# Optimization experiments

Hardware: AMD Instinct MI355X
Metric: run time of the kernel (lower is better)

The kernel has to match this reference:

```python
import jax, jax.numpy as jnp
import numpy as np

B, N = 32, 128
V, P, L = 50000, 40, 50
WD, UD = 100, 25
D = WD + UD          # 125: LSTM hidden per direction
H2 = 2 * D           # 250: BiLSTM output
HID = 100            # hidden_dim for scorers


def setup_inputs() -> dict:
    key = jax.random.key(0)
    ks = iter(jax.random.split(key, 40))
    p = lambda shape: jax.random.normal(next(ks), shape, jnp.float32) * 0.05
    inp = {
        'word_ids': jax.random.randint(next(ks), (B, N), 0, V),
        'upos_ids': jax.random.randint(next(ks), (B, N), 0, P),
        'target_arcs': jax.random.randint(next(ks), (B, N), 0, N),
        'wlookup': p((V, WD)),
        'tlookup': p((V, UD)),  # original sizes tag table by word_count
        # LSTM layer 0 (input D=125), layer 1 (input 2D=250); f=fwd, b=bwd dir
        'l0f_Wih': p((4 * D, D)), 'l0f_Whh': p((4 * D, D)), 'l0f_b': p((4 * D,)),
        'l0b_Wih': p((4 * D, D)), 'l0b_Whh': p((4 * D, D)), 'l0b_b': p((4 * D,)),
        'l1f_Wih': p((4 * D, H2)), 'l1f_Whh': p((4 * D, D)), 'l1f_b': p((4 * D,)),
        'l1b_Wih': p((4 * D, H2)), 'l1b_Whh': p((4 * D, D)), 'l1b_b': p((4 * D,)),
        'eh_W': p((HID, H2)), 'eh_b': p((HID,)),
        'em_W': p((HID, H2)), 'em_b': p((HID,)),
        'es_W': p((1, HID)), 'es_b': p((1,)),
        'lh_W': p((HID, H2)), 'lh_b': p((HID,)),
        'lm_W': p((HID, H2)), 'lm_b': p((HID,)),
        'ls_W': p((L, HID)), 'ls_b': p((L,)),
    }
    return inp


def _lstm_dir(x, Wih, Whh, b, reverse):
    # x: [B,T,in] -> h: [B,T,H], pytorch gate order i,f,g,o
    H = Whh.shape[1]
    xg = jnp.einsum('bti,gi->btg', x, Wih) + b  # precompute input projections

    def step(carry, xt):
        h, c = carry
        g = xt + h @ Whh.T
        i, f, gg, o = jnp.split(g, 4, axis=-1)
        c = jax.nn.sigmoid(f) * c + jax.nn.sigmoid(i) * jnp.tanh(gg)
        h = jax.nn.sigmoid(o) * jnp.tanh(c)
        return (h, c), h

    h0 = jnp.zeros((x.shape[0], H), x.dtype)
    _, hs = jax.lax.scan(step, (h0, h0), jnp.swapaxes(xg, 0, 1), reverse=reverse)
    return jnp.swapaxes(hs, 0, 1)


def _bilstm(x, Wf, Uf, bf, Wb, Ub, bb):
    return jnp.concatenate([_lstm_dir(x, Wf, Uf, bf, False),
                            _lstm_dir(x, Wb, Ub, bb, True)], axis=-1)


def reference(word_ids, upos_ids, target_arcs, wlookup, tlookup,
              l0f_Wih, l0f_Whh, l0f_b, l0b_Wih, l0b_Whh, l0b_b,
              l1f_Wih, l1f_Whh, l1f_b, l1b_Wih, l1b_Whh, l1b_b,
              eh_W, eh_b, em_W, em_b, es_W, es_b,
              lh_W, lh_b, lm_W, lm_b, ls_W, ls_b):
    n = word_ids.shape[1]
    words = jnp.concatenate([wlookup[word_ids], tlookup[upos_ids]], axis=-1)  # [B,N,125]
    h0 = _bilstm(words, l0f_Wih, l0f_Whh, l0f_b, l0b_Wih, l0b_Whh, l0b_b)
    word_exprs = _bilstm(h0, l1f_Wih, l1f_Whh, l1f_b, l1b_Wih, l1b_Whh, l1b_b)  # [B,N,250]

    word_h = word_exprs @ eh_W.T + eh_b  # [B,N,100]
    word_m = word_exprs @ em_W.T + em_b
    # fused pairwise biaffine-style scoring (replaces the O(n) python loop)
    pair = jnp.tanh(word_h[:, :, None, :] + word_m[:, None, :, :])  # [B,N,N,100]
    arc_scores = jnp.einsum('bijh,h->bij', pair, es_W[0]) + es_b[0]  # [B,N,N]

    # training path: margin augmentation
    target_arcs = target_arcs.at[:, 0].set(0)
    margin = 1.0 - jax.nn.one_hot(target_arcs, n, dtype=arc_scores.dtype)
    arc_scores = arc_scores + margin

    # decode() is an external MST decoder; greedy argmax stand-in
    parsed_trees = jnp.argmax(arc_scores, axis=-1)

    tree = target_arcs  # is_train path
    rel_heads = jnp.take_along_axis(word_exprs, tree[:, :, None], axis=1)  # [B,N,250]
    rel_heads = rel_heads @ lh_W.T + lh_b
    rel_mod = word_exprs @ lm_W.T + lm_b
    rel_scores = jnp.tanh(rel_mod + rel_heads) @ ls_W.T + ls_b  # [B,N,L]
    predicted_rels = jnp.argmax(rel_scores, axis=-1)
    return (parsed_trees, predicted_rels, arc_scores, rel_scores)
```

## Files before the change

### kernel.cpp

```cpp
#include <hip/hip_runtime.h>
#include <hip/hip_bf16.h>
#include <math.h>

#define B 32
#define N 128
#define BT (B*N)
#define WD 100
#define UD 25
#define D 125
#define G4 (4*D)
#define H2 (2*D)
#define HID 100
#define L 50

__device__ __forceinline__ float fast_tanh(float x) {
    float e = __expf(2.0f * x);
    return 1.0f - 2.0f / (e + 1.0f);
}
__device__ __forceinline__ float fast_sigmoid(float x) {
    return 1.0f / (1.0f + __expf(-x));
}
__device__ __forceinline__ float bcast_lane(float v, int k) {
    return __builtin_bit_cast(float, __builtin_amdgcn_readlane(__builtin_bit_cast(int, v), k));
}

#define REP64(X) \
 X(0) X(1) X(2) X(3) X(4) X(5) X(6) X(7) X(8) X(9) \
 X(10) X(11) X(12) X(13) X(14) X(15) X(16) X(17) X(18) X(19) \
 X(20) X(21) X(22) X(23) X(24) X(25) X(26) X(27) X(28) X(29) \
 X(30) X(31) X(32) X(33) X(34) X(35) X(36) X(37) X(38) X(39) \
 X(40) X(41) X(42) X(43) X(44) X(45) X(46) X(47) X(48) X(49) \
 X(50) X(51) X(52) X(53) X(54) X(55) X(56) X(57) X(58) X(59) \
 X(60) X(61) X(62) X(63)

struct TJob { const float* src; float* dst; int R, C, ldo, coff, tile0, tiles_x; };
struct TArgs { TJob j[12]; };

__global__ __launch_bounds__(256)
void setup_fused(TArgs a, int n_tr,
                 const int* __restrict__ wids, const int* __restrict__ uids,
                 const float* __restrict__ wl, const float* __restrict__ tl,
                 float* __restrict__ words,
                 const float* __restrict__ l0f_b, const float* __restrict__ l0b_b,
                 const float* __restrict__ l1f_b, const float* __restrict__ l1b_b,
                 const float* __restrict__ eh_b, const float* __restrict__ em_b,
                 const float* __restrict__ lm_b,
                 float* __restrict__ b_l0, float* __restrict__ b_l1,
                 float* __restrict__ b_s3,
                 float* __restrict__ p0, float* __restrict__ p1,
                 float* __restrict__ p2, float* __restrict__ p3) {
    __shared__ float tile[32][33];
    int bid = blockIdx.x;
    int tid = threadIdx.x;
    if (bid < n_tr) {
        int ji = 0;
        #pragma unroll
        for (int i = 1; i < 12; i++) if (bid >= a.j[i].tile0) ji = i;
        TJob jb = a.j[ji];
        int t = bid - jb.tile0;
        int tx = t % jb.tiles_x, ty = t / jb.tiles_x;
        int txx = tid & 31, tyy = tid >> 5;
        int k0 = tx*32, n0 = ty*32;
        #pragma unroll
        for (int dy = 0; dy < 32; dy += 8) {
            int n = n0 + tyy + dy, k = k0 + txx;
            if (n < jb.R && k < jb.C)
                tile[tyy+dy][txx] = jb.src[(size_t)n*jb.C + k];
        }
        __syncthreads();
        #pragma unroll
        for (int dy = 0; dy < 32; dy += 8) {
            int k = k0 + tyy + dy, n = n0 + txx;
            if (k < jb.C && n < jb.R)
                jb.dst[(size_t)k*jb.ldo + jb.coff + n] = tile[txx][tyy+dy];
        }
        return;
    }
    bid -= n_tr;
    if (bid < 2048) {
        int bt = bid*2 + (tid >> 7);
        int t = tid & 127;
        int wid = wids[bt], uid = uids[bt];
        if (t < WD)       words[bt*D + t] = wl[(size_t)wid*WD + t];
        else if (t < D)   words[bt*D + t] = tl[(size_t)uid*UD + (t - WD)];
        return;
    }
    bid -= 2048;
    if (bid < 9) {
        int t = bid*256 + tid;
        if (t < 500)        b_l0[t] = l0f_b[t];
        else if (t < 1000)  b_l0[t] = l0b_b[t-500];
        else if (t < 1500)  b_l1[t-1000] = l1f_b[t-1000];
        else if (t < 2000)  b_l1[t-1000] = l1b_b[t-1500];
        else if (t < 2100)  b_s3[t-2000] = eh_b[t-2000];
        else if (t < 2200)  b_s3[t-2000] = em_b[t-2100];
        else if (t < 2300)  b_s3[t-2000] = lm_b[t-2200];
        return;
    }
    bid -= 9;
    int e = bid*256 + tid;
    if (e < 6064) {
        int m = e / 1516, o = e % 1516;
        float* p = (m == 0) ? p0 : (m == 1) ? p1 : (m == 2) ? p2 : p3;
        p[125*500 + o] = 0.0f;
    }
}

#define MT 16
template<int CPT, int BD>
__device__ __forceinline__
void proj_body(const float* __restrict__ x, const float* __restrict__ WT,
               const float* __restrict__ bias, float* __restrict__ out,
               int Ncols, int K, int ldx, const int* __restrict__ gather_idx,
               int blk, float* xs) {
    int m0 = blk * MT;
    for (int e = threadIdx.x; e < MT * K; e += BD) {
        int r = e / K, k = e - r * K;
        int m = m0 + r;
        int row = m;
        if (gather_idx) {
            int bb = m >> 7, np = m & 127;
            row = (bb << 7) + (np == 0 ? 0 : gather_idx[m]);
        }
        xs[k*17 + r] = x[(size_t)row*ldx + k];
    }
    __syncthreads();
    int n0 = threadIdx.x;
    int lane = threadIdx.x & 63;
    float acc[CPT][MT];
    int ncl[CPT];
    #pragma unroll
    for (int j = 0; j < CPT; j++) {
        int n = n0 + j*BD;
        ncl[j] = (n < Ncols) ? n : (Ncols - 1);
        #pragma unroll
        for (int r = 0; r < MT; r++) acc[j][r] = 0.0f;
    }
    float wkc[4][CPT];
    #pragma unroll
    for (int q = 0; q < 4; q++)
        #pragma unroll
        for (int j = 0; j < CPT; j++)
            wkc[q][j] = WT[(size_t)q*Ncols + ncl[j]];
    int k0 = 0;
    for (; k0 + 8 <= K; k0 += 4) {
        float xv = xs[(k0 + (lane >> 4))*17 + (lane & 15)];
        float wkn[4][CPT];
        #pragma unroll
        for (int q = 0; q < 4; q++)
            #pragma unroll
            for (int j = 0; j < CPT; j++)
                wkn[q][j] = WT[(size_t)(k0 + 4 + q)*Ncols + ncl[j]];
        #pragma unroll
        for (int q = 0; q < 4; q++) {
            #pragma unroll
            for (int r = 0; r < 16; r++) {
                float hv = bcast_lane(xv, q*16 + r);
                #pragma unroll
                for (int j = 0; j < CPT; j++)
                    acc[j][r] = fmaf(wkc[q][j], hv, acc[j][r]);
            }
        }
        #pragma unroll
        for (int q = 0; q < 4; q++)
            #pragma unroll
            for (int j = 0; j < CPT; j++)
                wkc[q][j] = wkn[q][j];
    }
    {
        float xv = xs[(k0 + (lane >> 4))*17 + (lane & 15)];
        #pragma unroll
        for (int q = 0; q < 4; q++) {
            #pragma unroll
            for (int r = 0; r < 16; r++) {
                float hv = bcast_lane(xv, q*16 + r);
                #pragma unroll
                for (int j = 0; j < CPT; j++)
                    acc[j][r] = fmaf(wkc[q][j], hv, acc[j][r]);
            }
        }
        k0 += 4;
    }
    for (; k0 < K; k0++) {
        float xv = xs[k0*17 + (lane & 15)];
        float wk[CPT];
        #pragma unroll
        for (int j = 0; j < CPT; j++) wk[j] = WT[(size_t)k0*Ncols + ncl[j]];
        #pragma unroll
        for (int r = 0; r < 16; r++) {
            float hv = bcast_lane(xv, r);
            #pragma unroll
            for (int j = 0; j < CPT; j++)
                acc[j][r] = fmaf(wk[j], hv, acc[j][r]);
        }
    }
    #pragma unroll
    for (int j = 0; j < CPT; j++) {
        int n = n0 + j*BD;
        if (n < Ncols) {
            float bb = bias[n];
            #pragma unroll
            for (int r = 0; r < MT; r++) out[(size_t)(m0 + r)*Ncols + n] = acc[j][r] + bb;
        }
    }
}

__global__ __launch_bounds__(512)
void proj_t(const float* __restrict__ x, const float* __restrict__ WT,
            const float* __restrict__ bias, float* __restrict__ out,
            int Ncols, int K, int ldx) {
    __shared__ float xs[250 * 17 + 16];
    proj_body<2, 512>(x, WT, bias, out, Ncols, K, ldx, nullptr, blockIdx.x, xs);
}

__global__ __launch_bounds__(256)
void proj_s3lh(const float* __restrict__ x,
               const float* __restrict__ WTa, const float* __restrict__ ba,
               float* __restrict__ outa,
               const float* __restrict__ WTb, const float* __restrict__ bb,
               float* __restrict__ outb, const int* __restrict__ gather_idx) {
    __shared__ float xs[250 * 17 + 16];
    int job = blockIdx.x >> 8;
    int blk = blockIdx.x & 255;
    if (job == 0)
        proj_body<2, 256>(x, WTa, ba, outa, 300, H2, H2, nullptr, blk, xs);
    else
        proj_body<2, 256>(x, WTb, bb, outb, 100, H2, H2, gather_idx, blk, xs);
}

__global__ __launch_bounds__(1024, 4)
void lstm_scan(const float* __restrict__ xgc,
               const float* __restrict__ WhTf, const float* __restrict__ WhTb,
               float* __restrict__ out) {
    int dir = blockIdx.x & 1;
    int b = blockIdx.x >> 1;
    const float* WhT = dir ? WhTb : WhTf;
    int off = dir ? D : 0;
    int t = threadIdx.x;
    int g = t & 511;
    int half = t >> 9;
    int kbase = half << 6;

    __shared__ __align__(16) float hbuf[128];
    __shared__ float pbuf[1024];

    unsigned voff0 = ((unsigned)kbase * 500u + (unsigned)g) * 4u;
#define DECLW(i) float w##i; \
    asm volatile("global_load_dword %0, %1, %2" \
                 : "=v"(w##i) : "v"(voff0 + (unsigned)(i)*2000u), "s"(WhT));
    REP64(DECLW)
#undef DECLW
    asm volatile("s_waitcnt vmcnt(0)" ::: "memory");

    float c = 0.0f;
    if (t < 128) hbuf[t] = 0.0f;
    __syncthreads();

    const float* xb = xgc + (size_t)b * N * 1000 + dir * 500;
    bool xa = (half == 0) && (g < G4);
    float x_next = xa ? xb[(size_t)(dir ? (N-1) : 0) * 1000 + g] : 0.0f;

    const float4* h4q = ((const float4*)hbuf) + (kbase >> 2);

#define FMA4(q, i0, i1, i2, i3) { float4 hv = h4q[q]; \
    a4[0] = fmaf(w##i0, hv.x, a4[0]); \
    a4[1] = fmaf(w##i1, hv.y, a4[1]); \
    a4[2] = fmaf(w##i2, hv.z, a4[2]); \
    a4[3] = fmaf(w##i3, hv.w, a4[3]); }

    for (int ti = 0; ti < N; ti++) {
        int tt = dir ? (N-1-ti) : ti;
        float x_cur = x_next;
        float xn = 0.0f;
        if (xa && ti + 1 < N)
            xn = xb[(size_t)(dir ? (tt-1) : (tt+1)) * 1000 + g];
        float a4[4];
        a4[0] = x_cur; a4[1] = 0.0f; a4[2] = 0.0f; a4[3] = 0.0f;
        FMA4(0,  0,  1,  2,  3)  FMA4(1,  4,  5,  6,  7)
        FMA4(2,  8,  9, 10, 11)  FMA4(3, 12, 13, 14, 15)
        FMA4(4, 16, 17, 18, 19)  FMA4(5, 20, 21, 22, 23)
        FMA4(6, 24, 25, 26, 27)  FMA4(7, 28, 29, 30, 31)
        FMA4(8, 32, 33, 34, 35)  FMA4(9, 36, 37, 38, 39)
        FMA4(10, 40, 41, 42, 43) FMA4(11, 44, 45, 46, 47)
        FMA4(12, 48, 49, 50, 51) FMA4(13, 52, 53, 54, 55)
        FMA4(14, 56, 57, 58, 59) FMA4(15, 60, 61, 62, 63)
        x_next = xn;
        pbuf[t] = (a4[0] + a4[1]) + (a4[2] + a4[3]);
        __syncthreads();
        if (t < D) {
            float iv = pbuf[t]       + pbuf[512 + t];
            float fv = pbuf[D+t]     + pbuf[512 + D+t];
            float gv = pbuf[2*D+t]   + pbuf[512 + 2*D+t];
            float ov = pbuf[3*D+t]   + pbuf[512 + 3*D+t];
            float si = fast_sigmoid(iv);
            float sf = fast_sigmoid(fv);
            float so = fast_sigmoid(ov);
            c = sf * c + si * fast_tanh(gv);
            float h = so * fast_tanh(c);
            hbuf[t] = h;
            out[(size_t)(b*N + tt)*H2 + off + t] = h;
        }
        __syncthreads();
    }
#undef FMA4
}

#define ITILE 4
__global__ __launch_bounds__(128)
void arc_rel(const float* __restrict__ s3,
             const float* __restrict__ esW, const float* __restrict__ esb,
             const int* __restrict__ ta, const float* __restrict__ rh,
             const float* __restrict__ lsW, const float* __restrict__ lsb,
             float* __restrict__ arc_out, float* __restrict__ tree_out,
             float* __restrict__ rel_out, float* __restrict__ pred_out) {
    __shared__ float wms[128 * 101];
    __shared__ float whs[ITILE][HID];
    __shared__ float es[HID];
    __shared__ float sv[128];
    __shared__ int   si[128];
    int j = threadIdx.x;

    if (blockIdx.x < 1024) {
        int blk = blockIdx.x;
        int b = blk >> 5, it = blk & 31;
        for (int e = j; e < 128 * HID; e += 128) {
            int r = e / HID, h = e - r * HID;
            wms[r*101 + h] = s3[(size_t)(b*N + r)*300 + 100 + h];
        }
        for (int e = j; e < ITILE * HID; e += 128) {
            int ii = e / HID, h = e - ii * HID;
            whs[ii][h] = s3[(size_t)(b*N + it*ITILE + ii)*300 + h];
        }
        if (j < HID) es[j] = esW[j];
        __syncthreads();
        float eb = esb[0];
        const float* wmr = &wms[j * 101];
        for (int ii = 0; ii < ITILE; ii++) {
            int i = it * ITILE + ii;
            int bi = b * N + i;
            float acc = 0.0f;
            for (int h = 0; h < HID; h++)
                acc = fmaf(es[h], fast_tanh(whs[ii][h] + wmr[h]), acc);
            int tai = (i == 0) ? 0 : ta[bi];
            float score = acc + eb + 1.0f - ((j == tai) ? 1.0f : 0.0f);
            arc_out[(size_t)bi*N + j] = score;
            sv[j] = score; si[j] = j;
            __syncthreads();
            for (int s = 64; s; s >>= 1) {
                if (j < s) {
                    float ov = sv[j+s]; int oi = si[j+s];
                    if (ov > sv[j] || (ov == sv[j] && oi < si[j])) { sv[j] = ov; si[j] = oi; }
                }
                __syncthreads();
            }
            if (j == 0) tree_out[bi] = (float)si[0];
            __syncthreads();
        }
    } else {
        int bt = blockIdx.x - 1024;
        float* tv = es;
        if (j < HID)
            tv[j] = fast_tanh(s3[(size_t)bt*300 + 200 + j] + rh[(size_t)bt*HID + j]);
        __syncthreads();
        float score = -1e30f;
        if (j < L) {
            float acc = 0.0f;
            const float* wrow = lsW + j*HID;
            for (int h = 0; h < HID; h++) acc = fmaf(wrow[h], tv[h], acc);
            score = acc + lsb[j];
            rel_out[(size_t)bt*L + j] = score;
        }
        sv[j] = score; si[j] = j;
        __syncthreads();
        for (int s = 64; s; s >>= 1) {
            if (j < s) {
                float ov = sv[j+s]; int oi = si[j+s];
                if (ov > sv[j] || (ov == sv[j] && oi < si[j])) { sv[j] = ov; si[j] = oi; }
            }
            __syncthreads();
        }
        if (j == 0) pred_out[bt] = (float)si[0];
    }
}

extern "C" void kernel_launch(void* const* d_in, const int* in_sizes, int n_in,
                              void* d_out, int out_size, void* d_ws, size_t ws_size,
                              hipStream_t stream) {
    const int*   word_ids    = (const int*)  d_in[0];
    const int*   upos_ids    = (const int*)  d_in[1];
    const int*   target_arcs = (const int*)  d_in[2];
    const float* wlookup     = (const float*)d_in[3];
    const float* tlookup     = (const float*)d_in[4];
    const float* l0f_Wih = (const float*)d_in[5];
    const float* l0f_Whh = (const float*)d_in[6];
    const float* l0f_b   = (const float*)d_in[7];
    const float* l0b_Wih = (const float*)d_in[8];
    const float* l0b_Whh = (const float*)d_in[9];
    const float* l0b_b   = (const float*)d_in[10];
    const float* l1f_Wih = (const float*)d_in[11];
    const float* l1f_Whh = (const float*)d_in[12];
    const float* l1f_b   = (const float*)d_in[13];
    const float* l1b_Wih = (const float*)d_in[14];
    const float* l1b_Whh = (const float*)d_in[15];
    const float* l1b_b   = (const float*)d_in[16];
    const float* eh_W = (const float*)d_in[17];
    const float* eh_b = (const float*)d_in[18];
    const float* em_W = (const float*)d_in[19];
    const float* em_b = (const float*)d_in[20];
    const float* es_W = (const float*)d_in[21];
    const float* es_b = (const float*)d_in[22];
    const float* lh_W = (const float*)d_in[23];
    const float* lh_b = (const float*)d_in[24];
    const float* lm_W = (const float*)d_in[25];
    const float* lm_b = (const float*)d_in[26];
    const float* ls_W = (const float*)d_in[27];
    const float* ls_b = (const float*)d_in[28];

    float* out = (float*)d_out;
    float* trees_out = out;
    float* preds_out = out + BT;
    float* arc_out   = out + 2*BT;
    float* rel_out   = out + 2*BT + BT*N;

    float* ws = (float*)d_ws;
    float* A       = ws;
    float* words   = ws + 4096000;
    float* C       = ws + 4608000;
    float* WT_l0   = ws + 5632000;
    float* WT_l1   = ws + 5757000;
    float* WT_s3   = ws + 6007000;
    float* WT_lh   = ws + 6082000;
    float* WhT_l0f = ws + 6107000;
    float* WhT_l0b = ws + 6171016;
    float* WhT_l1f = ws + 6235032;
    float* WhT_l1b = ws + 6299048;
    float* b_l0    = ws + 6363064;
    float* b_l1    = ws + 6364064;
    float* b_s3    = ws + 6365064;
    float* rel_head = ws + 6366064;

    TArgs ta{};
    int n_tr = 0;
    {
        auto tiles = [](int R, int C_) { return ((C_+31)/32) * ((R+31)/32); };
        struct { const float* s; float* d; int R, C, ldo, coff; } js[12] = {
            { l0f_Wih, WT_l0, 500, 125, 1000, 0 },
            { l0b_Wih, WT_l0, 500, 125, 1000, 500 },
            { l1f_Wih, WT_l1, 500, 250, 1000, 0 },
            { l1b_Wih, WT_l1, 500, 250, 1000, 500 },
            { eh_W, WT_s3, 100, 250, 300, 0 },
            { em_W, WT_s3, 100, 250, 300, 100 },
            { lm_W, WT_s3, 100, 250, 300, 200 },
            { lh_W, WT_lh, 100, 250, 100, 0 },
            { l0f_Whh, WhT_l0f, 500, 125, 500, 0 },
            { l0b_Whh, WhT_l0b, 500, 125, 500, 0 },
            { l1f_Whh, WhT_l1f, 500, 125, 500, 0 },
            { l1b_Whh, WhT_l1b, 500, 125, 500, 0 },
        };
        for (int i = 0; i < 12; i++) {
            ta.j[i].src = js[i].s;  ta.j[i].dst = js[i].d;
            ta.j[i].R = js[i].R;    ta.j[i].C = js[i].C;
            ta.j[i].ldo = js[i].ldo; ta.j[i].coff = js[i].coff;
            ta.j[i].tile0 = n_tr;
            ta.j[i].tiles_x = (js[i].C + 31) / 32;
            n_tr += tiles(js[i].R, js[i].C);
        }
    }
    setup_fused<<<n_tr + 2048 + 9 + 24, 256, 0, stream>>>(
        ta, n_tr, word_ids, upos_ids, wlookup, tlookup, words,
        l0f_b, l0b_b, l1f_b, l1b_b, eh_b, em_b, lm_b,
        b_l0, b_l1, b_s3, WhT_l0f, WhT_l0b, WhT_l1f, WhT_l1b);

    proj_t<<<BT/MT, 512, 0, stream>>>(words, WT_l0, b_l0, A, 1000, D, D);

    lstm_scan<<<B*2, 1024, 0, stream>>>(A, WhT_l0f, WhT_l0b, C);

    proj_t<<<BT/MT, 512, 0, stream>>>(C, WT_l1, b_l1, A, 1000, H2, H2);

    lstm_scan<<<B*2, 1024, 0, stream>>>(A, WhT_l1f, WhT_l1b, C);

    proj_s3lh<<<512, 256, 0, stream>>>(C, WT_s3, b_s3, A,
                                       WT_lh, lh_b, rel_head, target_arcs);

    arc_rel<<<1024 + BT, 128, 0, stream>>>(A, es_W, es_b, target_arcs, rel_head,
                                           ls_W, ls_b, arc_out, trees_out,
                                           rel_out, preds_out);
}
```

Baseline: 594.2 us.

## Restructure LSTM recurrence to 512 threads with float4 weight tiles and lane broadcast

The recurrent LSTM scan now runs with 512 threads instead of 1024. Each thread holds a 32x4 float4 tile of the transposed recurrent weights and gets each hidden value through a readlane broadcast instead of LDS float4 reads. The K dimension is split four ways, so partial sums are reduced over four pbuf slices. The recurrent weight matrices are padded to a 512 stride, with the padding zeroed in setup, so the float4 loads stay aligned. This aims to cut LDS traffic and per-step barrier cost, but it adds more reduction adds and higher register pressure at 128 weight floats per thread.

```diff
diff --git a/kernel.cpp b/kernel.cpp
--- a/kernel.cpp
+++ b/kernel.cpp
@@ -23,15 +23,6 @@
 __device__ __forceinline__ float bcast_lane(float v, int k) {
     return __builtin_bit_cast(float, __builtin_amdgcn_readlane(__builtin_bit_cast(int, v), k));
 }
-
-#define REP64(X) \
- X(0) X(1) X(2) X(3) X(4) X(5) X(6) X(7) X(8) X(9) \
- X(10) X(11) X(12) X(13) X(14) X(15) X(16) X(17) X(18) X(19) \
- X(20) X(21) X(22) X(23) X(24) X(25) X(26) X(27) X(28) X(29) \
- X(30) X(31) X(32) X(33) X(34) X(35) X(36) X(37) X(38) X(39) \
- X(40) X(41) X(42) X(43) X(44) X(45) X(46) X(47) X(48) X(49) \
- X(50) X(51) X(52) X(53) X(54) X(55) X(56) X(57) X(58) X(59) \
- X(60) X(61) X(62) X(63)
 
 struct TJob { const float* src; float* dst; int R, C, ldo, coff, tile0, tiles_x; };
 struct TArgs { TJob j[12]; };
@@ -99,10 +90,16 @@
     }
     bid -= 9;
     int e = bid*256 + tid;
-    if (e < 6064) {
-        int m = e / 1516, o = e % 1516;
+    if (e < 12144) {
+        int m = e / 3036, o = e % 3036;
         float* p = (m == 0) ? p0 : (m == 1) ? p1 : (m == 2) ? p2 : p3;
-        p[125*500 + o] = 0.0f;
+        if (o < 1500) {
+            int k = o / 12, cc = 500 + (o % 12);
+            p[k*512 + cc] = 0.0f;
+        } else {
+            int o2 = o - 1500;
+            p[(125 + (o2 >> 9))*512 + (o2 & 511)] = 0.0f;
+        }
     }
 }
 
@@ -228,7 +225,7 @@
         proj_body<2, 256>(x, WTb, bb, outb, 100, H2, H2, gather_idx, blk, xs);
 }
 
-__global__ __launch_bounds__(1024, 4)
+__global__ __launch_bounds__(512)
 void lstm_scan(const float* __restrict__ xgc,
                const float* __restrict__ WhTf, const float* __restrict__ WhTb,
                float* __restrict__ out) {
@@ -237,61 +234,53 @@
     const float* WhT = dir ? WhTb : WhTf;
     int off = dir ? D : 0;
     int t = threadIdx.x;
-    int g = t & 511;
-    int half = t >> 9;
-    int kbase = half << 6;
+    int lane = t & 63;
+    int w = t >> 6;
+    int ks = w >> 1;
+    int cg = ((w & 1) << 6) + lane;
+    int c0 = cg << 2;
 
     __shared__ __align__(16) float hbuf[128];
-    __shared__ float pbuf[1024];
-
-    unsigned voff0 = ((unsigned)kbase * 500u + (unsigned)g) * 4u;
-#define DECLW(i) float w##i; \
-    asm volatile("global_load_dword %0, %1, %2" \
-                 : "=v"(w##i) : "v"(voff0 + (unsigned)(i)*2000u), "s"(WhT));
-    REP64(DECLW)
-#undef DECLW
-    asm volatile("s_waitcnt vmcnt(0)" ::: "memory");
-
-    float c = 0.0f;
+    __shared__ __align__(16) float pbuf[4*512];
+
+    float4 wv[32];
+    #pragma unroll
+    for (int k = 0; k < 32; k++)
+        wv[k] = *(const float4*)&WhT[(size_t)(ks*32 + k)*512 + c0];
+
     if (t < 128) hbuf[t] = 0.0f;
     __syncthreads();
 
     const float* xb = xgc + (size_t)b * N * 1000 + dir * 500;
-    bool xa = (half == 0) && (g < G4);
-    float x_next = xa ? xb[(size_t)(dir ? (N-1) : 0) * 1000 + g] : 0.0f;
-
-    const float4* h4q = ((const float4*)hbuf) + (kbase >> 2);
-
-#define FMA4(q, i0, i1, i2, i3) { float4 hv = h4q[q]; \
-    a4[0] = fmaf(w##i0, hv.x, a4[0]); \
-    a4[1] = fmaf(w##i1, hv.y, a4[1]); \
-    a4[2] = fmaf(w##i2, hv.z, a4[2]); \
-    a4[3] = fmaf(w##i3, hv.w, a4[3]); }
-
+    bool xa = (ks == 0) && (cg < 125);
+    float4 x_next = make_float4(0.f, 0.f, 0.f, 0.f);
+    if (xa) x_next = *(const float4*)&xb[(size_t)(dir ? (N-1) : 0)*1000 + c0];
+
+    float c = 0.0f;
     for (int ti = 0; ti < N; ti++) {
         int tt = dir ? (N-1-ti) : ti;
-        float x_cur = x_next;
-        float xn = 0.0f;
+        float vh = hbuf[ks*32 + (lane & 31)];
+        float4 x_cur = x_next;
+        float4 xn = make_float4(0.f, 0.f, 0.f, 0.f);
         if (xa && ti + 1 < N)
-            xn = xb[(size_t)(dir ? (tt-1) : (tt+1)) * 1000 + g];
-        float a4[4];
-        a4[0] = x_cur; a4[1] = 0.0f; a4[2] = 0.0f; a4[3] = 0.0f;
-        FMA4(0,  0,  1,  2,  3)  FMA4(1,  4,  5,  6,  7)
-        FMA4(2,  8,  9, 10, 11)  FMA4(3, 12, 13, 14, 15)
-        FMA4(4, 16, 17, 18, 19)  FMA4(5, 20, 21, 22, 23)
-        FMA4(6, 24, 25, 26, 27)  FMA4(7, 28, 29, 30, 31)
-        FMA4(8, 32, 33, 34, 35)  FMA4(9, 36, 37, 38, 39)
-        FMA4(10, 40, 41, 42, 43) FMA4(11, 44, 45, 46, 47)
-        FMA4(12, 48, 49, 50, 51) FMA4(13, 52, 53, 54, 55)
-        FMA4(14, 56, 57, 58, 59) FMA4(15, 60, 61, 62, 63)
+            xn = *(const float4*)&xb[(size_t)(dir ? (tt-1) : (tt+1))*1000 + c0];
+        float a0 = x_cur.x, a1 = x_cur.y, a2 = x_cur.z, a3 = x_cur.w;
+        #pragma unroll
+        for (int k = 0; k < 32; k++) {
+            float hs = bcast_lane(vh, k);
+            a0 = fmaf(wv[k].x, hs, a0);
+            a1 = fmaf(wv[k].y, hs, a1);
+            a2 = fmaf(wv[k].z, hs, a2);
+            a3 = fmaf(wv[k].w, hs, a3);
+        }
         x_next = xn;
-        pbuf[t] = (a4[0] + a4[1]) + (a4[2] + a4[3]);
+        *(float4*)&pbuf[ks*512 + c0] = make_float4(a0, a1, a2, a3);
         __syncthreads();
         if (t < D) {
-            float iv = pbuf[t]       + pbuf[512 + t];
-            float fv = pbuf[D+t]     + pbuf[512 + D+t];
-            float gv = pbuf[2*D+t]   + pbuf[512 + 2*D+t];
-            float ov = pbuf[3*D+t]   + pbuf[512 + 3*D+t];
+            float iv = pbuf[t]       + pbuf[512+t]       + pbuf[1024+t]       + pbuf[1536+t];
+            float fv = pbuf[125+t]   + pbuf[512+125+t]   + pbuf[1024+125+t]   + pbuf[1536+125+t];
+            float gv = pbuf[250+t]   + pbuf[512+250+t]   + pbuf[1024+250+t]   + pbuf[1536+250+t];
+            float ov = pbuf[375+t]   + pbuf[512+375+t]   + pbuf[1024+375+t]   + pbuf[1536+375+t];
             float si = fast_sigmoid(iv);
             float sf = fast_sigmoid(fv);
             float so = fast_sigmoid(ov);
@@ -302,7 +291,6 @@
         }
         __syncthreads();
     }
-#undef FMA4
 }
 
 #define ITILE 4
@@ -431,13 +419,13 @@
     float* WT_s3   = ws + 6007000;
     float* WT_lh   = ws + 6082000;
     float* WhT_l0f = ws + 6107000;
-    float* WhT_l0b = ws + 6171016;
-    float* WhT_l1f = ws + 6235032;
-    float* WhT_l1b = ws + 6299048;
-    float* b_l0    = ws + 6363064;
-    float* b_l1    = ws + 6364064;
-    float* b_s3    = ws + 6365064;
-    float* rel_head = ws + 6366064;
+    float* WhT_l0b = ws + 6172536;
+    float* WhT_l1f = ws + 6238072;
+    float* WhT_l1b = ws + 6303608;
+    float* b_l0    = ws + 6369144;
+    float* b_l1    = ws + 6370144;
+    float* b_s3    = ws + 6371144;
+    float* rel_head = ws + 6372144;
 
     TArgs ta{};
     int n_tr = 0;
@@ -452,10 +440,10 @@
             { em_W, WT_s3, 100, 250, 300, 100 },
             { lm_W, WT_s3, 100, 250, 300, 200 },
             { lh_W, WT_lh, 100, 250, 100, 0 },
-            { l0f_Whh, WhT_l0f, 500, 125, 500, 0 },
-            { l0b_Whh, WhT_l0b, 500, 125, 500, 0 },
-            { l1f_Whh, WhT_l1f, 500, 125, 500, 0 },
-            { l1b_Whh, WhT_l1b, 500, 125, 500, 0 },
+            { l0f_Whh, WhT_l0f, 500, 125, 512, 0 },
+            { l0b_Whh, WhT_l0b, 500, 125, 512, 0 },
+            { l1f_Whh, WhT_l1f, 500, 125, 512, 0 },
+            { l1b_Whh, WhT_l1b, 500, 125, 512, 0 },
         };
         for (int i = 0; i < 12; i++) {
             ta.j[i].src = js[i].s;  ta.j[i].dst = js[i].d;
@@ -466,18 +454,18 @@
             n_tr += tiles(js[i].R, js[i].C);
         }
     }
-    setup_fused<<<n_tr + 2048 + 9 + 24, 256, 0, stream>>>(
+    setup_fused<<<n_tr + 2048 + 9 + 48, 256, 0, stream>>>(
         ta, n_tr, word_ids, upos_ids, wlookup, tlookup, words,
         l0f_b, l0b_b, l1f_b, l1b_b, eh_b, em_b, lm_b,
         b_l0, b_l1, b_s3, WhT_l0f, WhT_l0b, WhT_l1f, WhT_l1b);
 
     proj_t<<<BT/MT, 512, 0, stream>>>(words, WT_l0, b_l0, A, 1000, D, D);
 
-    lstm_scan<<<B*2, 1024, 0, stream>>>(A, WhT_l0f, WhT_l0b, C);
+    lstm_scan<<<B*2, 512, 0, stream>>>(A, WhT_l0f, WhT_l0b, C);
 
     proj_t<<<BT/MT, 512, 0, stream>>>(C, WT_l1, b_l1, A, 1000, H2, H2);
 
-    lstm_scan<<<B*2, 1024, 0, stream>>>(A, WhT_l1f, WhT_l1b, C);
+    lstm_scan<<<B*2, 512, 0, stream>>>(A, WhT_l1f, WhT_l1b, C);
 
     proj_s3lh<<<512, 256, 0, stream>>>(C, WT_s3, b_s3, A,
                                        WT_lh, lh_b, rel_head, target_arcs);
```

After: 558.2 us. 1.06x faster.
